# Optimization experiments

Hardware: AMD Instinct MI355X
Metric: run time of the kernel (lower is better)

Reference implementation:

```python
import jax, jax.numpy as jnp
import numpy as np

N_NODES = 50000
N_EDGES = 1_600_000
N_RELS = 8
N_BASES = 4
H_DIM = 64


def setup_inputs() -> dict:
    key = jax.random.key(0)
    ks = jax.random.split(key, 12)
    return {
        "features": jax.random.normal(ks[0], (N_NODES, 2), dtype=jnp.float32),
        "src": jax.random.randint(ks[1], (N_EDGES,), 0, N_NODES),
        "dst": jax.random.randint(ks[2], (N_EDGES,), 0, N_NODES),
        "etype": jax.random.randint(ks[3], (N_EDGES,), 0, N_RELS),
        "W_in": jax.random.normal(ks[4], (2, H_DIM), dtype=jnp.float32) * 0.5,
        "b_in": jax.random.normal(ks[5], (H_DIM,), dtype=jnp.float32) * 0.1,
        "w_comp": jax.random.normal(ks[6], (N_RELS, N_BASES), dtype=jnp.float32) * 0.5,
        "bases": jax.random.normal(ks[7], (N_BASES, H_DIM, H_DIM), dtype=jnp.float32) * (1.0 / np.sqrt(H_DIM)),
        "loop_w": jax.random.normal(ks[8], (H_DIM, H_DIM), dtype=jnp.float32) * (1.0 / np.sqrt(H_DIM)),
        "h_bias": jax.random.normal(ks[9], (H_DIM,), dtype=jnp.float32) * 0.1,
        "fc_W": jax.random.normal(ks[10], (N_NODES * H_DIM, 1), dtype=jnp.float32) * (1.0 / np.sqrt(N_NODES * H_DIM)),
        "fc_b": jax.random.normal(ks[11], (1,), dtype=jnp.float32) * 0.1,
    }


def reference(features, src, dst, etype, W_in, b_in, w_comp, bases, loop_w, h_bias, fc_W, fc_b):
    n = features.shape[0]
    # Input embedding layer: Linear(2, h_dim) on node features
    h = features @ W_in + b_in                              # [N, d]
    # Basis-decomposed relation weights: W_r = sum_b w_comp[r,b] * bases[b]
    W = jnp.einsum('rb,bio->rio', w_comp, bases)            # [R, d, d]
    # Project all nodes under each relation (low_mem grouping equivalent)
    proj = jnp.einsum('ni,rio->rno', h, W)                  # [R, N, d]
    # Gather per-edge message, scatter-add to destination (sum aggregation, norm=None)
    msg = proj[etype, src]                                  # [E, d]
    agg = jax.ops.segment_sum(msg, dst, num_segments=n)     # [N, d]
    # Self-loop + bias, activation=None, dropout omitted (eval mode)
    out = agg + h @ loop_w + h_bias                         # [N, d]
    x = out.reshape(1, -1)                                  # [1, N*d]
    return jax.nn.sigmoid(x @ fc_W + fc_b)                  # [1, 1]
```

## Files before the change

kernel.cpp:

```cpp
#include <hip/hip_runtime.h>
#include <math.h>

#define N_NODES 50000
#define N_EDGES 1600000
#define N_RELS 8
#define N_BASES 4
#define HD 64

#define NB_D 196
#define NB_E 2048

#define G_OFF    0
#define PART_OFF 1728
#define D_OFF    4096

__global__ void prep_kernel(const float* __restrict__ W_in,
                            const float* __restrict__ b_in,
                            const float* __restrict__ w_comp,
                            const float* __restrict__ bases,
                            const float* __restrict__ loop_w,
                            const float* __restrict__ h_bias,
                            float* __restrict__ G) {
    __shared__ float sA[N_BASES * 3 * HD];
    const int tid = threadIdx.x;
    const int o = tid & 63;
    const int b = tid >> 6;

    {
        float s0 = 0.f, s1 = 0.f, sb = 0.f;
        for (int i = 0; i < HD; i++) {
            float bv = bases[b * HD * HD + i * HD + o];
            s0 += W_in[i]      * bv;
            s1 += W_in[HD + i] * bv;
            sb += b_in[i]      * bv;
        }
        sA[(b * 3 + 0) * HD + o] = s0;
        sA[(b * 3 + 1) * HD + o] = s1;
        sA[(b * 3 + 2) * HD + o] = sb;
    }
    __syncthreads();

    for (int idx = tid; idx < 24 * HD; idx += 256) {
        int j = idx >> 6, oo = idx & 63;
        int r = j / 3, k = j % 3;
        float s = 0.f;
#pragma unroll
        for (int bb = 0; bb < N_BASES; bb++)
            s += w_comp[r * N_BASES + bb] * sA[(bb * 3 + k) * HD + oo];
        G[j * HD + oo] = s;
    }

    if (tid < 3 * HD) {
        int k = tid >> 6, oo = tid & 63;
        float s = 0.f;
        for (int i = 0; i < HD; i++) {
            float w = (k == 0) ? W_in[i] : (k == 1) ? W_in[HD + i] : b_in[i];
            s += w * loop_w[i * HD + oo];
        }
        if (k == 2) s += h_bias[oo];
        G[(24 + k) * HD + oo] = s;
    }
}

__global__ __launch_bounds__(256) void d_table_kernel(
        const float4* __restrict__ fcW4,
        const float2* __restrict__ feat,
        const float* __restrict__ G,
        float* __restrict__ D,
        float* __restrict__ partD) {
    const int v = blockIdx.x * 256 + threadIdx.x;
    float part = 0.f;

    if (v < N_NODES) {
        float4 Fr[16];
#pragma unroll
        for (int k = 0; k < 16; k++) Fr[k] = fcW4[v * 16 + k];

        float s[27];
#pragma unroll
        for (int j = 0; j < 27; j++) {
            float acc = 0.f;
#pragma unroll
            for (int k = 0; k < 16; k++) {
                float gx = G[j * HD + 4 * k + 0];
                float gy = G[j * HD + 4 * k + 1];
                float gz = G[j * HD + 4 * k + 2];
                float gw = G[j * HD + 4 * k + 3];
                acc += Fr[k].x * gx + Fr[k].y * gy + Fr[k].z * gz + Fr[k].w * gw;
            }
            s[j] = acc;
        }

        float* dp = D + (size_t)v * 24;
#pragma unroll
        for (int j = 0; j < 24; j++) dp[j] = s[j];

        float2 f = feat[v];
        part = s[24] * f.x + s[25] * f.y + s[26];
    }

    __shared__ float red[256];
    red[threadIdx.x] = part;
    __syncthreads();
    for (int st = 128; st > 0; st >>= 1) {
        if (threadIdx.x < st) red[threadIdx.x] += red[threadIdx.x + st];
        __syncthreads();
    }
    if (threadIdx.x == 0) partD[blockIdx.x] = red[0];
}

__global__ __launch_bounds__(256) void edge_gather_kernel(
        const int* __restrict__ src,
        const int* __restrict__ dst,
        const int* __restrict__ et,
        const float2* __restrict__ feat,
        const float* __restrict__ D,
        float* __restrict__ partE) {
    float s = 0.f;
    const int stride = NB_E * 256;
    for (int e = blockIdx.x * 256 + threadIdx.x; e < N_EDGES; e += stride) {
        int u = src[e];
        int v = dst[e];
        int r = et[e];
        float2 f = feat[u];
        const float* dp = D + (size_t)v * 24 + r * 3;
        s += f.x * dp[0] + f.y * dp[1] + dp[2];
    }

    __shared__ float red[256];
    red[threadIdx.x] = s;
    __syncthreads();
    for (int st = 128; st > 0; st >>= 1) {
        if (threadIdx.x < st) red[threadIdx.x] += red[threadIdx.x + st];
        __syncthreads();
    }
    if (threadIdx.x == 0) partE[blockIdx.x] = red[0];
}

__global__ void final_kernel(const float* __restrict__ part,
                             const float* __restrict__ fc_b,
                             float* __restrict__ out) {
    float s = 0.f;
    for (int i = threadIdx.x; i < NB_D + NB_E; i += 256) s += part[i];
    __shared__ float red[256];
    red[threadIdx.x] = s;
    __syncthreads();
    for (int st = 128; st > 0; st >>= 1) {
        if (threadIdx.x < st) red[threadIdx.x] += red[threadIdx.x + st];
        __syncthreads();
    }
    if (threadIdx.x == 0) {
        float x = red[0] + fc_b[0];
        out[0] = 1.0f / (1.0f + expf(-x));
    }
}

extern "C" void kernel_launch(void* const* d_in, const int* in_sizes, int n_in,
                              void* d_out, int out_size, void* d_ws, size_t ws_size,
                              hipStream_t stream) {
    const float* features = (const float*)d_in[0];
    const int*   src      = (const int*)d_in[1];
    const int*   dst      = (const int*)d_in[2];
    const int*   etype    = (const int*)d_in[3];
    const float* W_in     = (const float*)d_in[4];
    const float* b_in     = (const float*)d_in[5];
    const float* w_comp   = (const float*)d_in[6];
    const float* bases    = (const float*)d_in[7];
    const float* loop_w   = (const float*)d_in[8];
    const float* h_bias   = (const float*)d_in[9];
    const float* fc_W     = (const float*)d_in[10];
    const float* fc_b     = (const float*)d_in[11];

    float* ws   = (float*)d_ws;
    float* G    = ws + G_OFF;
    float* part = ws + PART_OFF;
    float* D    = ws + D_OFF;
    float* out  = (float*)d_out;

    prep_kernel<<<1, 256, 0, stream>>>(W_in, b_in, w_comp, bases, loop_w, h_bias, G);
    d_table_kernel<<<NB_D, 256, 0, stream>>>(
        (const float4*)fc_W, (const float2*)features, G, D, part);
    edge_gather_kernel<<<NB_E, 256, 0, stream>>>(
        src, dst, etype, (const float2*)features, D, part + NB_D);
    final_kernel<<<1, 256, 0, stream>>>(part, fc_b, out);
}
```

Before: 151.2 us.

## Vectorize edge index loads and store D table as padded float4 per relation

The per-node D table is changed from 24 packed floats per node to a relation-major array of float4 entries, so each edge gather reads one aligned 16-byte value instead of three scalar loads. The edge kernel now processes four edges per thread using 128-bit nontemporal loads of src/dst/etype, and the block count is halved to match. This targets load instruction count and cache pollution from streaming index arrays, at the cost of a larger D table because of padding, and reads from relation planes that are farther apart in memory.

New measurement: 149.3 us. About the same (-1.3%).

```diff
diff --git a/kernel.cpp b/kernel.cpp
--- a/kernel.cpp
+++ b/kernel.cpp
@@ -8,7 +8,9 @@
 #define HD 64
 
 #define NB_D 196
-#define NB_E 2048
+#define NB_E 1024
+
+typedef int   vint4   __attribute__((ext_vector_type(4)));
 
 #define G_OFF    0
 #define PART_OFF 1728
@@ -66,7 +68,7 @@
         const float4* __restrict__ fcW4,
         const float2* __restrict__ feat,
         const float* __restrict__ G,
-        float* __restrict__ D,
+        float4* __restrict__ D,
         float* __restrict__ partD) {
     const int v = blockIdx.x * 256 + threadIdx.x;
     float part = 0.f;
@@ -91,9 +93,9 @@
             s[j] = acc;
         }
 
-        float* dp = D + (size_t)v * 24;
-#pragma unroll
-        for (int j = 0; j < 24; j++) dp[j] = s[j];
+#pragma unroll
+        for (int r = 0; r < N_RELS; r++)
+            D[r * N_NODES + v] = make_float4(s[3 * r], s[3 * r + 1], s[3 * r + 2], 0.f);
 
         float2 f = feat[v];
         part = s[24] * f.x + s[25] * f.y + s[26];
@@ -110,21 +112,34 @@
 }
 
 __global__ __launch_bounds__(256) void edge_gather_kernel(
-        const int* __restrict__ src,
-        const int* __restrict__ dst,
-        const int* __restrict__ et,
+        const vint4* __restrict__ src4,
+        const vint4* __restrict__ dst4,
+        const vint4* __restrict__ et4,
         const float2* __restrict__ feat,
-        const float* __restrict__ D,
+        const float4* __restrict__ D,
         float* __restrict__ partE) {
+    const int nquad = N_EDGES / 4;
+    const int stride = NB_E * 256;
     float s = 0.f;
-    const int stride = NB_E * 256;
-    for (int e = blockIdx.x * 256 + threadIdx.x; e < N_EDGES; e += stride) {
-        int u = src[e];
-        int v = dst[e];
-        int r = et[e];
-        float2 f = feat[u];
-        const float* dp = D + (size_t)v * 24 + r * 3;
-        s += f.x * dp[0] + f.y * dp[1] + dp[2];
+
+    for (int q = blockIdx.x * 256 + threadIdx.x; q < nquad; q += stride) {
+        vint4 u = __builtin_nontemporal_load(&src4[q]);
+        vint4 v = __builtin_nontemporal_load(&dst4[q]);
+        vint4 r = __builtin_nontemporal_load(&et4[q]);
+
+        float2 f0 = feat[u.x];
+        float2 f1 = feat[u.y];
+        float2 f2 = feat[u.z];
+        float2 f3 = feat[u.w];
+        float4 d0 = D[r.x * N_NODES + v.x];
+        float4 d1 = D[r.y * N_NODES + v.y];
+        float4 d2 = D[r.z * N_NODES + v.z];
+        float4 d3 = D[r.w * N_NODES + v.w];
+
+        s += f0.x * d0.x + f0.y * d0.y + d0.z;
+        s += f1.x * d1.x + f1.y * d1.y + d1.z;
+        s += f2.x * d2.x + f2.y * d2.y + d2.z;
+        s += f3.x * d3.x + f3.y * d3.y + d3.z;
     }
 
     __shared__ float red[256];
@@ -174,13 +189,14 @@
     float* ws   = (float*)d_ws;
     float* G    = ws + G_OFF;
     float* part = ws + PART_OFF;
-    float* D    = ws + D_OFF;
+    float4* D   = (float4*)(ws + D_OFF);
     float* out  = (float*)d_out;
 
     prep_kernel<<<1, 256, 0, stream>>>(W_in, b_in, w_comp, bases, loop_w, h_bias, G);
     d_table_kernel<<<NB_D, 256, 0, stream>>>(
         (const float4*)fc_W, (const float2*)features, G, D, part);
     edge_gather_kernel<<<NB_E, 256, 0, stream>>>(
-        src, dst, etype, (const float2*)features, D, part + NB_D);
+        (const vint4*)src, (const vint4*)dst, (const vint4*)etype,
+        (const float2*)features, D, part + NB_D);
     final_kernel<<<1, 256, 0, stream>>>(part, fc_b, out);
 }
```
